# Optimization experiments

Hardware: AMD Instinct MI355X
Metric: run time of the kernel (lower is better)

The kernel has to match this reference:

```python
import jax, jax.numpy as jnp
import numpy as np

N = 50000
HID = 128
NH = 4
E_RES, E_SEQ, E_KNN = 100000, 100000, 200000
BN_EPS = 1e-5
NEG_SLOPE = 0.2


def _gat(h, src, dst, W, al, ar, resW, b):
    """DGL-style GATConv (eval mode: feat_drop off, residual=True, bias).
    h: (N, in), W/resW: (in, H*out), al/ar: (H, out), b: (H*out,)"""
    Hh, out = al.shape
    feat = (h @ W).reshape(N, Hh, out)                 # (N, H, out)
    el = jnp.sum(feat * al, axis=-1)                   # (N, H)
    er = jnp.sum(feat * ar, axis=-1)                   # (N, H)
    e = jax.nn.leaky_relu(el[src] + er[dst], NEG_SLOPE)  # (E, H)
    # edge softmax over incoming edges of each dst node (numerically stable)
    m = jax.ops.segment_max(e, dst, num_segments=N)    # (N, H)
    ex = jnp.exp(e - m[dst])
    s = jax.ops.segment_sum(ex, dst, num_segments=N)
    a = ex / s[dst]                                    # (E, H)
    msg = a[:, :, None] * feat[src]                    # (E, H, out)
    rst = jax.ops.segment_sum(msg, dst, num_segments=N)  # (N, H, out)
    return rst + (h @ resW).reshape(N, Hh, out) + b.reshape(1, Hh, out)


def _hetero(h, src_res, dst_res, src_seq, dst_seq, src_knn, dst_knn, W, al, ar, resW, b):
    # HeteroGraphConv with aggregate='sum' over relations, then mean over heads
    r = _gat(h, src_res, dst_res, W[0], al[0], ar[0], resW[0], b[0])
    r = r + _gat(h, src_seq, dst_seq, W[1], al[1], ar[1], resW[1], b[1])
    r = r + _gat(h, src_knn, dst_knn, W[2], al[2], ar[2], resW[2], b[2])
    return jnp.mean(r, axis=1)                         # (N, out)


def setup_inputs() -> dict:
    key = jax.random.key(0)
    ks = iter(jax.random.split(key, 32))
    inp = {}
    inp["x"] = jax.random.normal(next(ks), (N, HID), jnp.float32)
    inp["src_res"] = jax.random.randint(next(ks), (E_RES,), 0, N, jnp.int32)
    inp["dst_res"] = jax.random.randint(next(ks), (E_RES,), 0, N, jnp.int32)
    inp["src_seq"] = jax.random.randint(next(ks), (E_SEQ,), 0, N, jnp.int32)
    inp["dst_seq"] = jax.random.randint(next(ks), (E_SEQ,), 0, N, jnp.int32)
    inp["src_knn"] = jax.random.randint(next(ks), (E_KNN,), 0, N, jnp.int32)
    inp["dst_knn"] = jax.random.randint(next(ks), (E_KNN,), 0, N, jnp.int32)
    sc = 0.05
    for l in (0, 1):
        inp[f"W{l}"] = jax.random.normal(next(ks), (3, HID, NH * HID), jnp.float32) * sc
        inp[f"al{l}"] = jax.random.normal(next(ks), (3, NH, HID), jnp.float32) * sc
        inp[f"ar{l}"] = jax.random.normal(next(ks), (3, NH, HID), jnp.float32) * sc
        inp[f"resW{l}"] = jax.random.normal(next(ks), (3, HID, NH * HID), jnp.float32) * sc
        inp[f"b{l}"] = jax.random.normal(next(ks), (3, NH * HID), jnp.float32) * sc
    inp["fc_W"] = jax.random.normal(next(ks), (HID, HID), jnp.float32) * sc
    inp["fc_b"] = jax.random.normal(next(ks), (HID,), jnp.float32) * sc
    inp["bn_gamma"] = jnp.ones((HID,), jnp.float32)
    inp["bn_beta"] = jnp.zeros((HID,), jnp.float32)
    inp["bn_mean"] = jax.random.normal(next(ks), (HID,), jnp.float32) * sc
    inp["bn_var"] = jax.random.uniform(next(ks), (HID,), jnp.float32)
    return inp


def reference(x, src_res, dst_res, src_seq, dst_seq, src_knn, dst_knn,
              W0, al0, ar0, resW0, b0, W1, al1, ar1, resW1, b1,
              fc_W, fc_b, bn_gamma, bn_beta, bn_mean, bn_var):
    # layer 0: hetero GAT, head-mean, fc + ReLU + BatchNorm (eval), dropout=identity
    h = _hetero(x, src_res, dst_res, src_seq, dst_seq, src_knn, dst_knn,
                W0, al0, ar0, resW0, b0)
    h = jax.nn.relu(h @ fc_W + fc_b)
    h = (h - bn_mean) / jnp.sqrt(bn_var + BN_EPS) * bn_gamma + bn_beta
    # layer 1 (final): hetero GAT, head-mean
    out = _hetero(h, src_res, dst_res, src_seq, dst_seq, src_knn, dst_knn,
                  W1, al1, ar1, resW1, b1)
    return out
```

## Files before the change

### kernel.cpp

```cpp
#include <hip/hip_runtime.h>
#include <hip/hip_bf16.h>
#include <math.h>
#include <stdint.h>

#define NNODES 50000
#define SCHUNK 4096
#define AW 1664
#define XOFF 1536

typedef __bf16 bf16x8 __attribute__((ext_vector_type(8)));
typedef float f32x4 __attribute__((ext_vector_type(4)));
typedef unsigned short u16;
typedef unsigned int u32;

__device__ __forceinline__ float lrelu(float x){ return x >= 0.f ? x : 0.2f*x; }
__device__ __forceinline__ float lo2f(u32 v){ union{ u32 i; float f; } c; c.i = v<<16; return c.f; }
__device__ __forceinline__ float hi2f(u32 v){ union{ u32 i; float f; } c; c.i = v & 0xffff0000u; return c.f; }
__device__ __forceinline__ u16 f2b(float f){ __hip_bfloat16 h = __float2bfloat16(f); return *(u16*)&h; }
__device__ __forceinline__ u32 packbf(float a, float b){ return (u32)f2b(a) | ((u32)f2b(b) << 16); }

#define GLDS16(g, l) __builtin_amdgcn_global_load_lds( \
    (const __attribute__((address_space(1))) void*)(g), \
    (__attribute__((address_space(3))) void*)(l), 16, 0, 0)

__global__ void prep_b(const float* __restrict__ W0, const float* __restrict__ W1,
                       const float* __restrict__ resW0, const float* __restrict__ resW1,
                       const float* __restrict__ b0, const float* __restrict__ b1,
                       u16* __restrict__ Btb, float* __restrict__ biasf)
{
    int gid = blockIdx.x*blockDim.x + threadIdx.x;
    if (gid < 2*128*AW){
        int l = gid / (128*AW);
        int rem = gid - l*(128*AW);
        int c = rem / AW;
        int j = rem - c*AW;
        const float* W  = l ? W1 : W0;
        const float* rw = l ? resW1 : resW0;
        float v;
        if (j < XOFF){
            int r = j >> 9, h = (j >> 7) & 3, k = j & 127;
            v = 0.25f * W[(size_t)r*65536 + (size_t)k*512 + h*128 + c];
        } else {
            int k = j - XOFF;
            float s = 0.f;
            for (int r = 0; r < 3; ++r)
                for (int h = 0; h < 4; ++h)
                    s += rw[(size_t)r*65536 + (size_t)k*512 + h*128 + c];
            v = 0.25f * s;
        }
        Btb[(size_t)l*128*AW + (size_t)(j>>3)*1024 + c*8 + (j&7)] = f2b(v);
    }
    if (gid < 256){
        int l = gid >> 7, c = gid & 127;
        const float* bb = l ? b1 : b0;
        float s = 0.f;
        for (int r = 0; r < 3; ++r)
            for (int h = 0; h < 4; ++h)
                s += bb[r*512 + h*128 + c];
        biasf[gid] = 0.25f*s;
    }
}

__global__ void prep_wl(const float* __restrict__ W0, const float* __restrict__ W1,
                        const float* __restrict__ al0, const float* __restrict__ ar0,
                        const float* __restrict__ al1, const float* __restrict__ ar1,
                        const float* __restrict__ fcW,
                        u16* __restrict__ wlb, u16* __restrict__ fcWtb)
{
    int gid = blockIdx.x*blockDim.x + threadIdx.x;
    if (gid < 2*128*128){
        int l = gid >> 14;
        int col = (gid >> 7) & 127;
        int k = gid & 127;
        float v = 0.f;
        if (col < 24){
            int r = col >> 3, lr = (col >> 2) & 1, h = col & 3;
            const float* W = l ? W1 : W0;
            const float* av = l ? (lr ? ar1 : al1) : (lr ? ar0 : al0);
            const float* wrow = W + (size_t)r*65536 + (size_t)k*512 + h*128;
            const float* arow = av + r*512 + h*128;
            for (int cc = 0; cc < 128; ++cc) v += wrow[cc]*arow[cc];
        }
        wlb[gid] = f2b(v);
    }
    if (gid < 128*128){
        int k = gid & 127, n = gid >> 7;
        fcWtb[gid] = f2b(fcW[k*128 + n]);
    }
}

__global__ __launch_bounds__(256) void xprep_kernel(const float* __restrict__ x,
    u16* __restrict__ Xg, const u16* __restrict__ wl, float* __restrict__ el, int M)
{
    __shared__ u16 Xs[64*136];
    __shared__ u16 Ws[32*136];
    const int tid = threadIdx.x;
    const int row0 = blockIdx.x*64;
    #pragma unroll
    for (int p = 0; p < 2; ++p){
        int idx = tid + p*256;
        int c = idx >> 4, kc = (idx & 15)*8;
        float4 v = make_float4(0.f,0.f,0.f,0.f);
        if (c < 24) v = *(const float4*)(wl + c*128 + kc);
        *(float4*)&Ws[c*136 + kc] = v;
    }
    int r = tid >> 2, cq = (tid & 3)*32;
    int grow = row0 + r;
    if (grow < M){
        #pragma unroll
        for (int i = 0; i < 8; ++i){
            float4 v = *(const float4*)(x + (size_t)grow*128 + cq + i*4);
            ushort4 o;
            o.x = f2b(v.x); o.y = f2b(v.y); o.z = f2b(v.z); o.w = f2b(v.w);
            *(ushort4*)(Xg + (size_t)grow*128 + cq + i*4) = o;
            *(ushort4*)&Xs[r*136 + cq + i*4] = o;
        }
    } else {
        ushort4 z; z.x=0; z.y=0; z.z=0; z.w=0;
        #pragma unroll
        for (int i = 0; i < 8; ++i) *(ushort4*)&Xs[r*136 + cq + i*4] = z;
    }
    __syncthreads();
    const int lane = tid & 63, wave = tid >> 6;
    const int r16 = lane & 15, quad = lane >> 4;
    f32x4 acc0 = {}, acc1 = {};
    #pragma unroll
    for (int ks = 0; ks < 4; ++ks){
        int ko = ks*32 + quad*8;
        bf16x8 a  = *(const bf16x8*)&Xs[(wave*16 + r16)*136 + ko];
        bf16x8 b0 = *(const bf16x8*)&Ws[r16*136 + ko];
        bf16x8 b1 = *(const bf16x8*)&Ws[(16 + r16)*136 + ko];
        acc0 = __builtin_amdgcn_mfma_f32_16x16x32_bf16(a, b0, acc0, 0,0,0);
        acc1 = __builtin_amdgcn_mfma_f32_16x16x32_bf16(a, b1, acc1, 0,0,0);
    }
    #pragma unroll
    for (int p = 0; p < 4; ++p){
        int row = row0 + wave*16 + quad*4 + p;
        if (row < M){
            el[(size_t)row*32 + r16] = acc0[p];
            if (r16 < 8) el[(size_t)row*32 + 16 + r16] = acc1[p];
        }
    }
}

__global__ void hist_all(const int* __restrict__ d0, const int* __restrict__ d1,
                         const int* __restrict__ d2, int e0, int e1, int e2,
                         int* __restrict__ cnt)
{
    int g = blockIdx.x*blockDim.x + threadIdx.x;
    if (g >= e0 + e1 + e2) return;
    int rel, idx;
    if (g < e0){ rel = 0; idx = g; }
    else if (g < e0 + e1){ rel = 1; idx = g - e0; }
    else { rel = 2; idx = g - e0 - e1; }
    const int* d = rel == 0 ? d0 : (rel == 1 ? d1 : d2);
    atomicAdd(cnt + (size_t)rel*NNODES + d[idx], 1);
}

__global__ __launch_bounds__(256) void scan_part(const int* __restrict__ cnt_all,
                                                 int* __restrict__ partials, int Nn, int nblk)
{
    int rel = blockIdx.y, blk = blockIdx.x;
    const int* cnt = cnt_all + (size_t)rel*Nn;
    int tid = threadIdx.x;
    int i0 = blk*SCHUNK + tid*16;
    int s = 0;
    #pragma unroll
    for (int k = 0; k < 4; ++k){
        int idx = i0 + k*4;
        if (idx + 3 < Nn){ int4 v = *(const int4*)(cnt + idx); s += v.x+v.y+v.z+v.w; }
        else { for (int j = 0; j < 4; ++j) if (idx+j < Nn) s += cnt[idx+j]; }
    }
    #pragma unroll
    for (int off = 1; off < 64; off <<= 1) s += __shfl_xor(s, off);
    __shared__ int ws[4];
    if ((tid & 63) == 0) ws[tid>>6] = s;
    __syncthreads();
    if (tid == 0) partials[rel*nblk + blk] = ws[0]+ws[1]+ws[2]+ws[3];
}

__global__ __launch_bounds__(256) void scan_write(const int* __restrict__ cnt_all,
                                                  const int* __restrict__ partials,
                                                  int* __restrict__ rp_all, int* __restrict__ cur_all,
                                                  int Nn, int nblk)
{
    int rel = blockIdx.y, blk = blockIdx.x;
    const int* cnt = cnt_all + (size_t)rel*Nn;
    int* rp  = rp_all  + (size_t)rel*(Nn+1);
    int* cur = cur_all + (size_t)rel*Nn;
    int tid = threadIdx.x;
    __shared__ int sOff;
    __shared__ int wsum[4];
    if (tid == 0){
        int o = 0;
        for (int b = 0; b < blk; ++b) o += partials[rel*nblk + b];
        sOff = o;
        if (blk == 0){
            int t = 0;
            for (int b = 0; b < nblk; ++b) t += partials[rel*nblk + b];
            rp[Nn] = t;
        }
    }
    int i0 = blk*SCHUNK + tid*16;
    int v[16];
    int s = 0;
    #pragma unroll
    for (int k = 0; k < 16; ++k){
        int idx = i0 + k;
        v[k] = (idx < Nn) ? cnt[idx] : 0;
        s += v[k];
    }
    int lane = tid & 63;
    int incl = s;
    #pragma unroll
    for (int off = 1; off < 64; off <<= 1){
        int t = __shfl_up(incl, off);
        if (lane >= off) incl += t;
    }
    if (lane == 63) wsum[tid>>6] = incl;
    __syncthreads();
    int woff = 0;
    for (int w = 0; w < (tid>>6); ++w) woff += wsum[w];
    int ex = sOff + woff + incl - s;
    #pragma unroll
    for (int k = 0; k < 16; ++k){
        int idx = i0 + k;
        if (idx < Nn){ rp[idx] = ex; cur[idx] = ex; }
        ex += v[k];
    }
}

__global__ void scatter_all(const int* __restrict__ s0, const int* __restrict__ s1,
                            const int* __restrict__ s2,
                            const int* __restrict__ d0, const int* __restrict__ d1,
                            const int* __restrict__ d2, int e0, int e1, int e2,
                            int* __restrict__ cur, int* __restrict__ colb,
                            int* __restrict__ dste)
{
    int g = blockIdx.x*blockDim.x + threadIdx.x;
    if (g >= e0 + e1 + e2) return;
    int rel, idx, coff;
    if (g < e0){ rel = 0; idx = g; coff = 0; }
    else if (g < e0 + e1){ rel = 1; idx = g - e0; coff = e0; }
    else { rel = 2; idx = g - e0 - e1; coff = e0 + e1; }
    const int* sp = rel == 0 ? s0 : (rel == 1 ? s1 : s2);
    const int* dp = rel == 0 ? d0 : (rel == 1 ? d1 : d2);
    int d = dp[idx];
    int pos = atomicAdd(cur + (size_t)rel*NNODES + d, 1);
    colb[coff + pos] = sp[idx];
    dste[coff + pos] = d;
}

__global__ void wprep(const int* __restrict__ colb, const int* __restrict__ dste,
                      int e0, int e01, int etot,
                      const float* __restrict__ el_all, uint4* __restrict__ rec)
{
    int j = blockIdx.x*blockDim.x + threadIdx.x;
    if (j >= etot) return;
    int rel = (j < e0) ? 0 : ((j < e01) ? 1 : 2);
    int src = colb[j], dst = dste[j];
    float4 es = *(const float4*)(el_all + (size_t)src*32 + rel*8);
    float4 ed = *(const float4*)(el_all + (size_t)dst*32 + rel*8 + 4);
    uint4 o;
    o.x = (u32)src;
    o.y = packbf(__expf(lrelu(es.x + ed.x)), __expf(lrelu(es.y + ed.y)));
    o.z = packbf(__expf(lrelu(es.z + ed.z)), __expf(lrelu(es.w + ed.w)));
    o.w = 0;
    rec[j] = o;
}

template<int EPI>
__global__ __launch_bounds__(256, 2) void fused_gat(
    const int* __restrict__ rowp_all, const uint4* __restrict__ rec_all,
    int e0, int e01,
    const u16* __restrict__ Xg, const u16* __restrict__ Btg,
    float* __restrict__ Cf, u16* __restrict__ Cb, int M,
    const float* __restrict__ bias)
{
    __shared__ u16 smem[8192];
    const int tid = threadIdx.x;
    const int lane = tid & 63, wave = tid >> 6;
    const int r16 = lane & 15, quad = lane >> 4;
    const int row0 = blockIdx.x*64;
    const int nd = row0 + wave*16 + r16;

    f32x4 cacc[8] = {};
    bf16x8 afrag[16];

    #define STAGEB(buf, t) do { \
        const u16* s0_ = Btg + (size_t)(t)*4096; \
        GLDS16(s0_ + tid*8,        smem + (buf)*4096 + wave*512); \
        GLDS16(s0_ + 2048 + tid*8, smem + (buf)*4096 + 2048 + wave*512); \
    } while(0)

    STAGEB(0, 0);

    for (int r = 0; r < 3; ++r){
        const int* rp = rowp_all + (size_t)r*(NNODES+1);
        int beg = 0, end = 0;
        if (nd < M){ beg = rp[nd]; end = rp[nd+1]; }
        const int coff = (r == 0) ? 0 : ((r == 1) ? e0 : e01);
        const uint4* rc = rec_all + coff;
        float ac[4][4][8] = {};
        float us0 = 0.f, us1 = 0.f, us2 = 0.f, us3 = 0.f;
        uint4 ra = {0,0,0,0};
        uint4 p0 = {0,0,0,0}, p1 = {0,0,0,0}, p2 = {0,0,0,0}, p3 = {0,0,0,0};
        if (beg < end){
            ra = rc[beg];
            const u16* xr = Xg + (size_t)ra.x*128 + quad*8;
            p0 = *(const uint4*)(xr);      p1 = *(const uint4*)(xr + 32);
            p2 = *(const uint4*)(xr + 64); p3 = *(const uint4*)(xr + 96);
        }
        for (int j = beg; j < end; ++j){
            uint4 rb = ra, q0 = p0, q1 = p1, q2 = p2, q3 = p3;
            if (j + 1 < end){
                rb = rc[j+1];
                const u16* xr = Xg + (size_t)rb.x*128 + quad*8;
                q0 = *(const uint4*)(xr);      q1 = *(const uint4*)(xr + 32);
                q2 = *(const uint4*)(xr + 64); q3 = *(const uint4*)(xr + 96);
            }
            float w0 = lo2f(ra.y), w1 = hi2f(ra.y), w2 = lo2f(ra.z), w3 = hi2f(ra.z);
            us0 += w0; us1 += w1; us2 += w2; us3 += w3;
            #define PROCM(m, pv) do { \
                float xv[8]; \
                xv[0]=lo2f(pv.x); xv[1]=hi2f(pv.x); xv[2]=lo2f(pv.y); xv[3]=hi2f(pv.y); \
                xv[4]=lo2f(pv.z); xv[5]=hi2f(pv.z); xv[6]=lo2f(pv.w); xv[7]=hi2f(pv.w); \
                _Pragma("unroll") \
                for (int c = 0; c < 8; ++c){ \
                    ac[0][m][c] = fmaf(w0, xv[c], ac[0][m][c]); \
                    ac[1][m][c] = fmaf(w1, xv[c], ac[1][m][c]); \
                    ac[2][m][c] = fmaf(w2, xv[c], ac[2][m][c]); \
                    ac[3][m][c] = fmaf(w3, xv[c], ac[3][m][c]); \
                } \
            } while(0)
            PROCM(0, p0); PROCM(1, p1); PROCM(2, p2); PROCM(3, p3);
            #undef PROCM
            ra = rb; p0 = q0; p1 = q1; p2 = q2; p3 = q3;
        }
        float ivs[4];
        ivs[0] = us0 > 0.f ? 1.f/us0 : 0.f;
        ivs[1] = us1 > 0.f ? 1.f/us1 : 0.f;
        ivs[2] = us2 > 0.f ? 1.f/us2 : 0.f;
        ivs[3] = us3 > 0.f ? 1.f/us3 : 0.f;
        #pragma unroll
        for (int h = 0; h < 4; ++h){
            #pragma unroll
            for (int m = 0; m < 4; ++m){
                union { bf16x8 v; u32 w[4]; } u;
                u.w[0] = packbf(ac[h][m][0]*ivs[h], ac[h][m][1]*ivs[h]);
                u.w[1] = packbf(ac[h][m][2]*ivs[h], ac[h][m][3]*ivs[h]);
                u.w[2] = packbf(ac[h][m][4]*ivs[h], ac[h][m][5]*ivs[h]);
                u.w[3] = packbf(ac[h][m][6]*ivs[h], ac[h][m][7]*ivs[h]);
                afrag[h*4 + m] = u.v;
            }
        }
        if (r == 0) __syncthreads();
        #pragma unroll
        for (int m2 = 0; m2 < 16; ++m2){
            STAGEB((m2+1)&1, r*16 + m2 + 1);
            const u16* Bs = smem + (m2&1)*4096 + quad*1024;
            #pragma unroll
            for (int j = 0; j < 8; ++j){
                bf16x8 b = *(const bf16x8*)&Bs[(j*16 + r16)*8];
                cacc[j] = __builtin_amdgcn_mfma_f32_16x16x32_bf16(afrag[m2], b, cacc[j], 0,0,0);
            }
            __syncthreads();
        }
    }
    {
        int xrow = nd < M ? nd : M - 1;
        const u16* xr = Xg + (size_t)xrow*128 + quad*8;
        bf16x8 xf0 = *(const bf16x8*)(xr);
        bf16x8 xf1 = *(const bf16x8*)(xr + 32);
        bf16x8 xf2 = *(const bf16x8*)(xr + 64);
        bf16x8 xf3 = *(const bf16x8*)(xr + 96);
        #pragma unroll
        for (int m2 = 0; m2 < 4; ++m2){
            if (m2 < 3) STAGEB((m2+1)&1, 49 + m2);
            const u16* Bs = smem + (m2&1)*4096 + quad*1024;
            bf16x8 a = m2 == 0 ? xf0 : (m2 == 1 ? xf1 : (m2 == 2 ? xf2 : xf3));
            #pragma unroll
            for (int j = 0; j < 8; ++j){
                bf16x8 b = *(const bf16x8*)&Bs[(j*16 + r16)*8];
                cacc[j] = __builtin_amdgcn_mfma_f32_16x16x32_bf16(a, b, cacc[j], 0,0,0);
            }
            __syncthreads();
        }
    }
    #undef STAGEB
    #pragma unroll
    for (int j = 0; j < 8; ++j){
        int col = j*16 + r16;
        float bi = bias[col];
        #pragma unroll
        for (int p = 0; p < 4; ++p){
            int row = row0 + wave*16 + quad*4 + p;
            if (row < M){
                float v = cacc[j][p] + bi;
                if (EPI == 1) Cf[(size_t)row*128 + col] = v;
                else          Cb[(size_t)row*128 + col] = f2b(v);
            }
        }
    }
}

template<int EPI, int ELR>
__global__ __launch_bounds__(256) void gemm_f(
    const u16* __restrict__ A, int Astride, int K,
    const u16* __restrict__ Bt,
    float* __restrict__ Cf, u16* __restrict__ Cb, int Cstride, int M,
    const float* __restrict__ bias, const float* __restrict__ gamma,
    const float* __restrict__ beta, const float* __restrict__ mean,
    const float* __restrict__ var,
    const u16* __restrict__ wl, float* __restrict__ el)
{
    __shared__ u16 smem[24576];
    const int tid = threadIdx.x;
    const int row0 = blockIdx.x*64;
    const int lane = tid & 63, wave = tid >> 6;
    const int wm = (wave >> 1)*32, wn = (wave & 1)*64;
    const int r16 = lane & 15, quad = lane >> 4;
    const int swzbase = r16 & 7;
    f32x4 acc[2][4] = {};

    const int r8 = lane >> 3, jc = lane & 7;
    const int soff = ((jc ^ r8) << 3);
    int gA0 = row0 + wave*16 + r8;      if (gA0 >= M) gA0 = M - 1;
    int gA1 = row0 + wave*16 + 8 + r8;  if (gA1 >= M) gA1 = M - 1;
    const u16* srcA0 = A + (size_t)gA0*Astride + soff;
    const u16* srcA1 = A + (size_t)gA1*Astride + soff;
    const u16* srcB0 = Bt + (size_t)(wave*32      + r8)*K + soff;
    const u16* srcB1 = Bt + (size_t)(wave*32 + 8  + r8)*K + soff;
    const u16* srcB2 = Bt + (size_t)(wave*32 + 16 + r8)*K + soff;
    const u16* srcB3 = Bt + (size_t)(wave*32 + 24 + r8)*K + soff;
    const int nk = K >> 6;

    #define STAGE(buf, k0) do { \
        u16* As_ = smem + (buf)*12288; \
        u16* Bs_ = As_ + 4096; \
        GLDS16(srcA0 + (k0), As_ + wave*1024); \
        GLDS16(srcA1 + (k0), As_ + wave*1024 + 512); \
        GLDS16(srcB0 + (k0), Bs_ + wave*2048); \
        GLDS16(srcB1 + (k0), Bs_ + wave*2048 + 512); \
        GLDS16(srcB2 + (k0), Bs_ + wave*2048 + 1024); \
        GLDS16(srcB3 + (k0), Bs_ + wave*2048 + 1536); \
    } while (0)

    STAGE(0, 0);
    __syncthreads();
    for (int t = 0; t < nk; ++t){
        int cur = t & 1;
        if (t + 1 < nk) STAGE(cur ^ 1, (t + 1) << 6);
        const u16* As = smem + cur*12288;
        const u16* Bs = As + 4096;
        #pragma unroll
        for (int ks = 0; ks < 2; ++ks){
            int swz = ((ks*4 + quad) ^ swzbase) << 3;
            bf16x8 a0 = *(const bf16x8*)&As[(wm + r16)*64 + swz];
            bf16x8 a1 = *(const bf16x8*)&As[(wm + 16 + r16)*64 + swz];
            #pragma unroll
            for (int j = 0; j < 4; ++j){
                bf16x8 b = *(const bf16x8*)&Bs[(wn + j*16 + r16)*64 + swz];
                acc[0][j] = __builtin_amdgcn_mfma_f32_16x16x32_bf16(a0, b, acc[0][j], 0,0,0);
                acc[1][j] = __builtin_amdgcn_mfma_f32_16x16x32_bf16(a1, b, acc[1][j], 0,0,0);
            }
        }
        __syncthreads();
    }
    #undef STAGE

    u16* Cs = smem;
    u16* Ws = smem + 64*136;
    if (ELR){
        #pragma unroll
        for (int p = 0; p < 2; ++p){
            int idx = tid + p*256;
            int c = idx >> 4, kc = (idx & 15)*8;
            float4 v = make_float4(0.f,0.f,0.f,0.f);
            if (c < 24) v = *(const float4*)(wl + c*128 + kc);
            *(float4*)&Ws[c*136 + kc] = v;
        }
    }
    #pragma unroll
    for (int i = 0; i < 2; ++i){
        #pragma unroll
        for (int p = 0; p < 4; ++p){
            int rl = wm + i*16 + quad*4 + p;
            int row = row0 + rl;
            #pragma unroll
            for (int j = 0; j < 4; ++j){
                int col = wn + j*16 + r16;
                float v = acc[i][j][p] + bias[col];
                if (EPI == 2){
                    float t = fmaxf(v, 0.f);
                    v = (t - mean[col]) * rsqrtf(var[col] + 1e-5f) * gamma[col] + beta[col];
                }
                u16 vb = f2b(v);
                if (row < M){
                    if (EPI == 1) Cf[(size_t)row*Cstride + col] = v;
                    else          Cb[(size_t)row*Cstride + col] = vb;
                }
                if (ELR) Cs[rl*136 + col] = vb;
            }
        }
    }
    if (ELR){
        __syncthreads();
        f32x4 e0 = {}, e1 = {};
        #pragma unroll
        for (int ks = 0; ks < 4; ++ks){
            int ko = ks*32 + quad*8;
            bf16x8 a  = *(const bf16x8*)&Cs[(wave*16 + r16)*136 + ko];
            bf16x8 b0 = *(const bf16x8*)&Ws[r16*136 + ko];
            bf16x8 b1 = *(const bf16x8*)&Ws[(16 + r16)*136 + ko];
            e0 = __builtin_amdgcn_mfma_f32_16x16x32_bf16(a, b0, e0, 0,0,0);
            e1 = __builtin_amdgcn_mfma_f32_16x16x32_bf16(a, b1, e1, 0,0,0);
        }
        #pragma unroll
        for (int p = 0; p < 4; ++p){
            int row = row0 + wave*16 + quad*4 + p;
            if (row < M){
                el[(size_t)row*32 + r16] = e0[p];
                if (r16 < 8) el[(size_t)row*32 + 16 + r16] = e1[p];
            }
        }
    }
}

static inline char* align256(char* p){ return (char*)(((uintptr_t)p + 255) & ~(uintptr_t)255); }

extern "C" void kernel_launch(void* const* d_in, const int* in_sizes, int n_in,
                              void* d_out, int out_size, void* d_ws, size_t ws_size,
                              hipStream_t stream)
{
    const float* x      = (const float*)d_in[0];
    const int* srcs[3]  = {(const int*)d_in[1], (const int*)d_in[3], (const int*)d_in[5]};
    const int* dsts[3]  = {(const int*)d_in[2], (const int*)d_in[4], (const int*)d_in[6]};
    const int  E[3]     = {in_sizes[1], in_sizes[3], in_sizes[5]};
    const float* W0     = (const float*)d_in[7];
    const float* al0    = (const float*)d_in[8];
    const float* ar0    = (const float*)d_in[9];
    const float* resW0  = (const float*)d_in[10];
    const float* b0     = (const float*)d_in[11];
    const float* W1     = (const float*)d_in[12];
    const float* al1    = (const float*)d_in[13];
    const float* ar1    = (const float*)d_in[14];
    const float* resW1  = (const float*)d_in[15];
    const float* b1     = (const float*)d_in[16];
    const float* fcW    = (const float*)d_in[17];
    const float* fcb    = (const float*)d_in[18];
    const float* gamma  = (const float*)d_in[19];
    const float* beta   = (const float*)d_in[20];
    const float* bmean  = (const float*)d_in[21];
    const float* bvar   = (const float*)d_in[22];
    float* out = (float*)d_out;

    char* p = (char*)d_ws;
    u16*   Xg    = (u16*)p;   p += (size_t)NNODES*128*2;   p = align256(p);
    u16*   hx1   = (u16*)p;   p += (size_t)NNODES*128*2;   p = align256(p);
    u16*   hmb   = (u16*)p;   p += (size_t)NNODES*128*2;   p = align256(p);
    float* el    = (float*)p; p += (size_t)NNODES*32*4;    p = align256(p);
    int*   cnt   = (int*)p;   p += (size_t)3*NNODES*4;     p = align256(p);
    int*   rowp  = (int*)p;   p += (size_t)3*(NNODES+1)*4; p = align256(p);
    int*   cur   = (int*)p;   p += (size_t)3*NNODES*4;     p = align256(p);
    int*   colb  = (int*)p;   p += (size_t)(E[0]+E[1]+E[2])*4; p = align256(p);
    int*   dste  = (int*)p;   p += (size_t)(E[0]+E[1]+E[2])*4; p = align256(p);
    uint4* rec   = (uint4*)p; p += (size_t)(E[0]+E[1]+E[2])*16; p = align256(p);
    u16*   Btb   = (u16*)p;   p += (size_t)2*128*AW*2;     p = align256(p);
    u16*   wlb   = (u16*)p;   p += (size_t)2*128*128*2;    p = align256(p);
    u16*   fcWtb = (u16*)p;   p += (size_t)128*128*2;      p = align256(p);
    float* biasf = (float*)p; p += (size_t)2*128*4;        p = align256(p);
    int*   parts = (int*)p;   p += (size_t)3*64*4;

    const int NBLK = (NNODES + SCHUNK - 1)/SCHUNK;
    const int MB = (NNODES + 63)/64;
    const int ETOT = E[0] + E[1] + E[2];
    dim3 blk(256);

    hipMemsetAsync(cnt, 0, (size_t)3*NNODES*sizeof(int), stream);
    prep_b <<<(2*128*AW + 255)/256, blk, 0, stream>>>(W0, W1, resW0, resW1, b0, b1, Btb, biasf);
    prep_wl<<<(2*128*128 + 255)/256, blk, 0, stream>>>(W0, W1, al0, ar0, al1, ar1, fcW, wlb, fcWtb);
    xprep_kernel<<<MB, blk, 0, stream>>>(x, Xg, wlb, el, NNODES);
    hist_all<<<(ETOT + 255)/256, blk, 0, stream>>>(dsts[0], dsts[1], dsts[2], E[0], E[1], E[2], cnt);
    scan_part <<<dim3(NBLK,3), blk, 0, stream>>>(cnt, parts, NNODES, NBLK);
    scan_write<<<dim3(NBLK,3), blk, 0, stream>>>(cnt, parts, rowp, cur, NNODES, NBLK);
    scatter_all<<<(ETOT + 255)/256, blk, 0, stream>>>(srcs[0], srcs[1], srcs[2],
                                                      dsts[0], dsts[1], dsts[2],
                                                      E[0], E[1], E[2], cur, colb, dste);

    wprep<<<(ETOT + 255)/256, blk, 0, stream>>>(colb, dste, E[0], E[0]+E[1], ETOT, el, rec);
    fused_gat<4><<<MB, blk, 0, stream>>>(rowp, rec, E[0], E[0]+E[1], Xg, Btb,
                                         nullptr, hmb, NNODES, biasf);
    gemm_f<2,1><<<MB, blk, 0, stream>>>(hmb, 128, 128, fcWtb, nullptr, hx1, 128, NNODES,
                                        fcb, gamma, beta, bmean, bvar, wlb + 16384, el);

    wprep<<<(ETOT + 255)/256, blk, 0, stream>>>(colb, dste, E[0], E[0]+E[1], ETOT, el, rec);
    fused_gat<1><<<MB, blk, 0, stream>>>(rowp, rec, E[0], E[0]+E[1], hx1, Btb + (size_t)128*AW,
                                         out, nullptr, NNODES, biasf + 128);
}
```

Measured before the change: 396.3 us.

## Split fused GAT aggregation across 16 lanes per node and stage via LDS

The fused GAT kernel now gives each destination node's neighbor aggregation to 16 threads, each owning 8 feature columns, instead of one thread holding all 128 columns times 4 heads in registers. Aggregated rows are written to a swizzled LDS tile and then read back as MFMA A-fragments. Blocks cover 32 rows, with each wave computing a 16x64 output quadrant. This is meant to cut register pressure (launch bounds raised to 3 blocks per SM), improve gather coalescing, and spread skewed degree imbalance across more lanes. In exchange it adds LDS traffic and extra barriers, and each block re-stages the full weight matrix for half as many rows.

```diff
diff --git a/kernel.cpp b/kernel.cpp
--- a/kernel.cpp
+++ b/kernel.cpp
@@ -270,133 +270,140 @@
 }
 
 template<int EPI>
-__global__ __launch_bounds__(256, 2) void fused_gat(
+__global__ __launch_bounds__(256, 3) void fused_gat2(
     const int* __restrict__ rowp_all, const uint4* __restrict__ rec_all,
     int e0, int e01,
     const u16* __restrict__ Xg, const u16* __restrict__ Btg,
     float* __restrict__ Cf, u16* __restrict__ Cb, int M,
     const float* __restrict__ bias)
 {
-    __shared__ u16 smem[8192];
+    __shared__ u16 Atile[32*512];
+    __shared__ u16 Bbuf[2*4096];
     const int tid = threadIdx.x;
     const int lane = tid & 63, wave = tid >> 6;
     const int r16 = lane & 15, quad = lane >> 4;
-    const int row0 = blockIdx.x*64;
-    const int nd = row0 + wave*16 + r16;
-
-    f32x4 cacc[8] = {};
-    bf16x8 afrag[16];
-
-    #define STAGEB(buf, t) do { \
+    const int row0 = blockIdx.x*32;
+    const int mrow = (wave >> 1)*16;
+    const int ncol = (wave & 1)*64;
+    const int g = tid >> 4, o = tid & 15;
+    char* Ab = (char*)Atile;
+    f32x4 cacc[4] = {};
+    bf16x8 xfrag[4];
+
+    #define STAGEB2(buf, t) do { \
         const u16* s0_ = Btg + (size_t)(t)*4096; \
-        GLDS16(s0_ + tid*8,        smem + (buf)*4096 + wave*512); \
-        GLDS16(s0_ + 2048 + tid*8, smem + (buf)*4096 + 2048 + wave*512); \
+        GLDS16(s0_ + tid*8,        Bbuf + (buf)*4096 + wave*512); \
+        GLDS16(s0_ + 2048 + tid*8, Bbuf + (buf)*4096 + 2048 + wave*512); \
     } while(0)
 
-    STAGEB(0, 0);
+    STAGEB2(0, 0);
 
     for (int r = 0; r < 3; ++r){
         const int* rp = rowp_all + (size_t)r*(NNODES+1);
-        int beg = 0, end = 0;
-        if (nd < M){ beg = rp[nd]; end = rp[nd+1]; }
         const int coff = (r == 0) ? 0 : ((r == 1) ? e0 : e01);
         const uint4* rc = rec_all + coff;
-        float ac[4][4][8] = {};
-        float us0 = 0.f, us1 = 0.f, us2 = 0.f, us3 = 0.f;
-        uint4 ra = {0,0,0,0};
-        uint4 p0 = {0,0,0,0}, p1 = {0,0,0,0}, p2 = {0,0,0,0}, p3 = {0,0,0,0};
-        if (beg < end){
-            ra = rc[beg];
-            const u16* xr = Xg + (size_t)ra.x*128 + quad*8;
-            p0 = *(const uint4*)(xr);      p1 = *(const uint4*)(xr + 32);
-            p2 = *(const uint4*)(xr + 64); p3 = *(const uint4*)(xr + 96);
-        }
-        for (int j = beg; j < end; ++j){
-            uint4 rb = ra, q0 = p0, q1 = p1, q2 = p2, q3 = p3;
-            if (j + 1 < end){
-                rb = rc[j+1];
-                const u16* xr = Xg + (size_t)rb.x*128 + quad*8;
-                q0 = *(const uint4*)(xr);      q1 = *(const uint4*)(xr + 32);
-                q2 = *(const uint4*)(xr + 64); q3 = *(const uint4*)(xr + 96);
-            }
-            float w0 = lo2f(ra.y), w1 = hi2f(ra.y), w2 = lo2f(ra.z), w3 = hi2f(ra.z);
-            us0 += w0; us1 += w1; us2 += w2; us3 += w3;
-            #define PROCM(m, pv) do { \
-                float xv[8]; \
-                xv[0]=lo2f(pv.x); xv[1]=hi2f(pv.x); xv[2]=lo2f(pv.y); xv[3]=hi2f(pv.y); \
-                xv[4]=lo2f(pv.z); xv[5]=hi2f(pv.z); xv[6]=lo2f(pv.w); xv[7]=hi2f(pv.w); \
-                _Pragma("unroll") \
-                for (int c = 0; c < 8; ++c){ \
-                    ac[0][m][c] = fmaf(w0, xv[c], ac[0][m][c]); \
-                    ac[1][m][c] = fmaf(w1, xv[c], ac[1][m][c]); \
-                    ac[2][m][c] = fmaf(w2, xv[c], ac[2][m][c]); \
-                    ac[3][m][c] = fmaf(w3, xv[c], ac[3][m][c]); \
-                } \
-            } while(0)
-            PROCM(0, p0); PROCM(1, p1); PROCM(2, p2); PROCM(3, p3);
-            #undef PROCM
-            ra = rb; p0 = q0; p1 = q1; p2 = q2; p3 = q3;
-        }
-        float ivs[4];
-        ivs[0] = us0 > 0.f ? 1.f/us0 : 0.f;
-        ivs[1] = us1 > 0.f ? 1.f/us1 : 0.f;
-        ivs[2] = us2 > 0.f ? 1.f/us2 : 0.f;
-        ivs[3] = us3 > 0.f ? 1.f/us3 : 0.f;
-        #pragma unroll
-        for (int h = 0; h < 4; ++h){
+        #pragma unroll
+        for (int i = 0; i < 2; ++i){
+            const int row = g*2 + i;
+            const int nd = row0 + row;
+            int beg = 0, end = 0;
+            if (nd < M){ beg = rp[nd]; end = rp[nd+1]; }
+            float ac[4][8] = {};
+            float us0 = 0.f, us1 = 0.f, us2 = 0.f, us3 = 0.f;
+            uint4 ra; ra.x = 0; ra.y = 0; ra.z = 0; ra.w = 0;
+            uint4 xa; xa.x = 0; xa.y = 0; xa.z = 0; xa.w = 0;
+            if (beg < end){
+                ra = rc[beg];
+                xa = *(const uint4*)(Xg + (size_t)ra.x*128 + o*8);
+            }
+            for (int j = beg; j < end; ++j){
+                uint4 rb = ra, xb = xa;
+                if (j + 1 < end){
+                    rb = rc[j+1];
+                    xb = *(const uint4*)(Xg + (size_t)rb.x*128 + o*8);
+                }
+                float w0 = lo2f(ra.y), w1 = hi2f(ra.y), w2 = lo2f(ra.z), w3 = hi2f(ra.z);
+                us0 += w0; us1 += w1; us2 += w2; us3 += w3;
+                float xv[8];
+                xv[0] = lo2f(xa.x); xv[1] = hi2f(xa.x);
+                xv[2] = lo2f(xa.y); xv[3] = hi2f(xa.y);
+                xv[4] = lo2f(xa.z); xv[5] = hi2f(xa.z);
+                xv[6] = lo2f(xa.w); xv[7] = hi2f(xa.w);
+                #pragma unroll
+                for (int c = 0; c < 8; ++c){
+                    ac[0][c] = fmaf(w0, xv[c], ac[0][c]);
+                    ac[1][c] = fmaf(w1, xv[c], ac[1][c]);
+                    ac[2][c] = fmaf(w2, xv[c], ac[2][c]);
+                    ac[3][c] = fmaf(w3, xv[c], ac[3][c]);
+                }
+                ra = rb; xa = xb;
+            }
+            float ivs[4];
+            ivs[0] = us0 > 0.f ? 1.f/us0 : 0.f;
+            ivs[1] = us1 > 0.f ? 1.f/us1 : 0.f;
+            ivs[2] = us2 > 0.f ? 1.f/us2 : 0.f;
+            ivs[3] = us3 > 0.f ? 1.f/us3 : 0.f;
+            const u32 swz = ((u32)(row & 7)) << 4;
             #pragma unroll
-            for (int m = 0; m < 4; ++m){
-                union { bf16x8 v; u32 w[4]; } u;
-                u.w[0] = packbf(ac[h][m][0]*ivs[h], ac[h][m][1]*ivs[h]);
-                u.w[1] = packbf(ac[h][m][2]*ivs[h], ac[h][m][3]*ivs[h]);
-                u.w[2] = packbf(ac[h][m][4]*ivs[h], ac[h][m][5]*ivs[h]);
-                u.w[3] = packbf(ac[h][m][6]*ivs[h], ac[h][m][7]*ivs[h]);
-                afrag[h*4 + m] = u.v;
-            }
-        }
-        if (r == 0) __syncthreads();
+            for (int h = 0; h < 4; ++h){
+                uint4 ov;
+                ov.x = packbf(ac[h][0]*ivs[h], ac[h][1]*ivs[h]);
+                ov.y = packbf(ac[h][2]*ivs[h], ac[h][3]*ivs[h]);
+                ov.z = packbf(ac[h][4]*ivs[h], ac[h][5]*ivs[h]);
+                ov.w = packbf(ac[h][6]*ivs[h], ac[h][7]*ivs[h]);
+                *(uint4*)(Ab + (((u32)row*1024 + (u32)h*256 + (u32)o*16) ^ swz)) = ov;
+            }
+        }
+        __syncthreads();
+
+        if (r == 2){
+            int nd = row0 + mrow + r16; if (nd >= M) nd = M - 1;
+            const u16* xr = Xg + (size_t)nd*128 + quad*8;
+            xfrag[0] = *(const bf16x8*)(xr);
+            xfrag[1] = *(const bf16x8*)(xr + 32);
+            xfrag[2] = *(const bf16x8*)(xr + 64);
+            xfrag[3] = *(const bf16x8*)(xr + 96);
+        }
+
+        const u32 arswz = ((u32)((mrow + r16) & 7)) << 4;
+        const u32 arbase = (u32)(mrow + r16)*1024 + (u32)quad*16;
         #pragma unroll
         for (int m2 = 0; m2 < 16; ++m2){
-            STAGEB((m2+1)&1, r*16 + m2 + 1);
-            const u16* Bs = smem + (m2&1)*4096 + quad*1024;
+            int t = r*16 + m2;
+            STAGEB2((t+1)&1, t+1);
+            bf16x8 a = *(const bf16x8*)(Ab + ((arbase + (u32)m2*64) ^ arswz));
+            const u16* Bs = Bbuf + (t&1)*4096 + quad*1024 + ncol*8;
             #pragma unroll
-            for (int j = 0; j < 8; ++j){
-                bf16x8 b = *(const bf16x8*)&Bs[(j*16 + r16)*8];
-                cacc[j] = __builtin_amdgcn_mfma_f32_16x16x32_bf16(afrag[m2], b, cacc[j], 0,0,0);
+            for (int jj = 0; jj < 4; ++jj){
+                bf16x8 b = *(const bf16x8*)&Bs[(jj*16 + r16)*8];
+                cacc[jj] = __builtin_amdgcn_mfma_f32_16x16x32_bf16(a, b, cacc[jj], 0,0,0);
             }
             __syncthreads();
         }
     }
-    {
-        int xrow = nd < M ? nd : M - 1;
-        const u16* xr = Xg + (size_t)xrow*128 + quad*8;
-        bf16x8 xf0 = *(const bf16x8*)(xr);
-        bf16x8 xf1 = *(const bf16x8*)(xr + 32);
-        bf16x8 xf2 = *(const bf16x8*)(xr + 64);
-        bf16x8 xf3 = *(const bf16x8*)(xr + 96);
-        #pragma unroll
-        for (int m2 = 0; m2 < 4; ++m2){
-            if (m2 < 3) STAGEB((m2+1)&1, 49 + m2);
-            const u16* Bs = smem + (m2&1)*4096 + quad*1024;
-            bf16x8 a = m2 == 0 ? xf0 : (m2 == 1 ? xf1 : (m2 == 2 ? xf2 : xf3));
-            #pragma unroll
-            for (int j = 0; j < 8; ++j){
-                bf16x8 b = *(const bf16x8*)&Bs[(j*16 + r16)*8];
-                cacc[j] = __builtin_amdgcn_mfma_f32_16x16x32_bf16(a, b, cacc[j], 0,0,0);
-            }
-            __syncthreads();
-        }
-    }
-    #undef STAGEB
-    #pragma unroll
-    for (int j = 0; j < 8; ++j){
-        int col = j*16 + r16;
+    #pragma unroll
+    for (int m2 = 0; m2 < 4; ++m2){
+        int t = 48 + m2;
+        if (m2 < 3) STAGEB2((t+1)&1, t+1);
+        const u16* Bs = Bbuf + (t&1)*4096 + quad*1024 + ncol*8;
+        bf16x8 a = xfrag[m2];
+        #pragma unroll
+        for (int jj = 0; jj < 4; ++jj){
+            bf16x8 b = *(const bf16x8*)&Bs[(jj*16 + r16)*8];
+            cacc[jj] = __builtin_amdgcn_mfma_f32_16x16x32_bf16(a, b, cacc[jj], 0,0,0);
+        }
+        __syncthreads();
+    }
+    #undef STAGEB2
+    #pragma unroll
+    for (int jj = 0; jj < 4; ++jj){
+        int col = ncol + jj*16 + r16;
         float bi = bias[col];
         #pragma unroll
         for (int p = 0; p < 4; ++p){
-            int row = row0 + wave*16 + quad*4 + p;
+            int row = row0 + mrow + quad*4 + p;
             if (row < M){
-                float v = cacc[j][p] + bi;
+                float v = cacc[jj][p] + bi;
                 if (EPI == 1) Cf[(size_t)row*128 + col] = v;
                 else          Cb[(size_t)row*128 + col] = f2b(v);
             }
@@ -574,6 +581,7 @@
 
     const int NBLK = (NNODES + SCHUNK - 1)/SCHUNK;
     const int MB = (NNODES + 63)/64;
+    const int MB2 = (NNODES + 31)/32;
     const int ETOT = E[0] + E[1] + E[2];
     dim3 blk(256);
 
@@ -589,12 +597,12 @@
                                                       E[0], E[1], E[2], cur, colb, dste);
 
     wprep<<<(ETOT + 255)/256, blk, 0, stream>>>(colb, dste, E[0], E[0]+E[1], ETOT, el, rec);
-    fused_gat<4><<<MB, blk, 0, stream>>>(rowp, rec, E[0], E[0]+E[1], Xg, Btb,
-                                         nullptr, hmb, NNODES, biasf);
+    fused_gat2<4><<<MB2, blk, 0, stream>>>(rowp, rec, E[0], E[0]+E[1], Xg, Btb,
+                                           nullptr, hmb, NNODES, biasf);
     gemm_f<2,1><<<MB, blk, 0, stream>>>(hmb, 128, 128, fcWtb, nullptr, hx1, 128, NNODES,
                                         fcb, gamma, beta, bmean, bvar, wlb + 16384, el);
 
     wprep<<<(ETOT + 255)/256, blk, 0, stream>>>(colb, dste, E[0], E[0]+E[1], ETOT, el, rec);
-    fused_gat<1><<<MB, blk, 0, stream>>>(rowp, rec, E[0], E[0]+E[1], hx1, Btb + (size_t)128*AW,
-                                         out, nullptr, NNODES, biasf + 128);
-}
+    fused_gat2<1><<<MB2, blk, 0, stream>>>(rowp, rec, E[0], E[0]+E[1], hx1, Btb + (size_t)128*AW,
+                                           out, nullptr, NNODES, biasf + 128);
+}
```

Result: slower. 467.9 us (+18.1%).
